# Kernel tuning notes

Measured on AMD Instinct MI355X. Metric: run time of the kernel, lower is better.

## Reference

```python
import jax, jax.numpy as jnp
import numpy as np

N = 100000      # num nodes
T = 4           # num edge types
E = 150000      # edges per edge type
HID = 128       # hidden_dim
NH = 8          # num_heads
D = 16          # per_head_dim
MS = NH * D     # message size


def setup_inputs() -> dict:
    key = jax.random.key(0)
    ks = jax.random.split(key, 6)
    x = jax.random.normal(ks[0], (N, HID), dtype=jnp.float32)
    adj = jax.random.randint(ks[1], (T, E, 2), 0, N, dtype=jnp.int32)
    Wq = jax.random.normal(ks[2], (T, HID, MS), dtype=jnp.float32) * 0.05
    Wk = jax.random.normal(ks[3], (T, HID, MS), dtype=jnp.float32) * 0.05
    Wm = jax.random.normal(ks[4], (T, 2 * HID, MS), dtype=jnp.float32) * 0.05
    bm = jnp.zeros((T, MS), dtype=jnp.float32)
    return {"x": x, "adj": adj, "Wq": Wq, "Wk": Wk, "Wm": Wm, "bm": bm}


def reference(x, adj, Wq, Wk, Wm, bm):
    scale = D ** (-0.5)
    srcs = adj[..., 0]  # [T, E]
    tgts = adj[..., 1]  # [T, E]
    xs = x[srcs]        # [T, E, HID] gather
    xt = x[tgts]        # [T, E, HID] gather
    # per-edge-type message MLP (depth 1 -> single linear + relu)
    feats = jnp.concatenate([xs, xt], axis=-1)                 # [T, E, 2*HID]
    msgs = jax.nn.relu(jnp.einsum('tef,tfm->tem', feats, Wm) + bm[:, None, :])
    msgs = msgs.reshape(T * E, NH, D)
    # per-edge-type Q/K projections and per-head dot-product scores
    q = (scale * jnp.einsum('teh,thm->tem', xt, Wq)).reshape(T * E, NH, D)
    k = jnp.einsum('teh,thm->tem', xs, Wk).reshape(T * E, NH, D)
    scores = jnp.einsum('ehd,ehd->eh', q, k)                   # [T*E, NH]
    idx = tgts.reshape(-1)                                     # [T*E]
    # segment (scatter) softmax over edges grouped by target node
    m = jax.ops.segment_max(scores, idx, num_segments=N)       # [N, NH]
    m = jnp.where(jnp.isfinite(m), m, jnp.zeros_like(m))       # empty segments
    e = jnp.exp(scores - m[idx])
    denom = jax.ops.segment_sum(e, idx, num_segments=N)        # [N, NH]
    probs = e / denom[idx]                                     # [T*E, NH]
    # weighted scatter-sum aggregation
    agg = jax.ops.segment_sum(probs[..., None] * msgs, idx, num_segments=N)
    return agg.reshape(N, MS)
```

## Files before the change

### kernel.cpp

```cpp
#include <hip/hip_runtime.h>
#include <hip/hip_bf16.h>
#include <cstdint>

#define NND 100000
#define NT 4
#define NE 150000
#define TOTE (NT * NE)
#define HID 128
#define NHD 8
#define MS 128
#define SEL ((size_t)NND * MS)
#define BAT 8
#define PNW 32

typedef __bf16 bf16x8 __attribute__((ext_vector_type(8)));
typedef float f32x4 __attribute__((ext_vector_type(4)));

__device__ __forceinline__ float bf2f(unsigned int u16) {
  unsigned int b = u16 << 16;
  return __builtin_bit_cast(float, b);
}
__device__ __forceinline__ unsigned short f2bf(float f) {
  unsigned int b = __builtin_bit_cast(unsigned int, f);
  b += 0x7FFFu + ((b >> 16) & 1u);
  return (unsigned short)(b >> 16);
}

__global__ void k_convert_x(const float* __restrict__ x, unsigned short* __restrict__ xb) {
  int i = (blockIdx.x * 256 + threadIdx.x) * 4;
  float4 v = *reinterpret_cast<const float4*>(x + i);
  ushort4 o;
  o.x = f2bf(v.x); o.y = f2bf(v.y); o.z = f2bf(v.z); o.w = f2bf(v.w);
  *reinterpret_cast<ushort4*>(xb + i) = o;
}

__global__ void k_pack_w(const float* __restrict__ Wq, const float* __restrict__ Wk,
                         const float* __restrict__ Wm, unsigned short* __restrict__ wp) {
  int p = blockIdx.x * 256 + threadIdx.x;
  int e    = p & 7;
  int lane = (p >> 3) & 63;
  int b    = (p >> 9) & 3;
  int c    = (p >> 11) & 7;
  int kind = (p >> 14) & 3;
  int t    = p >> 16;
  int col = c * 16 + (lane & 15);
  int k   = b * 32 + (lane >> 4) * 8 + e;
  float v;
  if (kind == 0)      v = 0.25f * Wq[((size_t)t * HID + k) * MS + col];
  else if (kind == 1) v = Wk[((size_t)t * HID + k) * MS + col];
  else if (kind == 2) v = Wm[((size_t)t * 2 * HID + k) * MS + col];
  else                v = Wm[((size_t)t * 2 * HID + HID + k) * MS + col];
  wp[p] = f2bf(v);
}

__global__ void k_hist(const int* __restrict__ adj, int* __restrict__ counts) {
  int i = blockIdx.x * 256 + threadIdx.x;
  if (i < TOTE) atomicAdd(&counts[adj[2 * i + 1]], 1);
}

__global__ void k_blocksum(const int* __restrict__ counts, int* __restrict__ bsum) {
  __shared__ int s[4];
  int i = blockIdx.x * 256 + threadIdx.x;
  int v = (i < NND) ? counts[i] : 0;
#pragma unroll
  for (int d = 1; d < 64; d <<= 1) v += __shfl_xor(v, d);
  if ((threadIdx.x & 63) == 0) s[threadIdx.x >> 6] = v;
  __syncthreads();
  if (threadIdx.x == 0) bsum[blockIdx.x] = s[0] + s[1] + s[2] + s[3];
}

__global__ void k_scan_mid(int* __restrict__ bsum, int nb, int* __restrict__ offsets) {
  __shared__ int s[512];
  int t = threadIdx.x;
  s[t] = (t < nb) ? bsum[t] : 0;
  __syncthreads();
  for (int d = 1; d < 512; d <<= 1) {
    int u = (t >= d) ? s[t - d] : 0;
    __syncthreads();
    s[t] += u;
    __syncthreads();
  }
  if (t < nb) bsum[t] = (t > 0) ? s[t - 1] : 0;
  if (t == 0) offsets[NND] = TOTE;
}

__global__ void k_scan_add(const int* __restrict__ counts, const int* __restrict__ bsum,
                           int* __restrict__ offsets, int* __restrict__ cursor) {
  __shared__ int s[256];
  int b = blockIdx.x, t = threadIdx.x, i = b * 256 + t;
  s[t] = (i < NND) ? counts[i] : 0;
  __syncthreads();
  for (int d = 1; d < 256; d <<= 1) {
    int u = (t >= d) ? s[t - d] : 0;
    __syncthreads();
    s[t] += u;
    __syncthreads();
  }
  int excl = ((t > 0) ? s[t - 1] : 0) + bsum[b];
  if (i < NND) { offsets[i] = excl; cursor[i] = excl; }
}

__global__ void k_scatter(const int* __restrict__ adj, int* __restrict__ cursor,
                          int* __restrict__ edata) {
  int i = blockIdx.x * 256 + threadIdx.x;
  if (i >= TOTE) return;
  int src = adj[2 * i], tgt = adj[2 * i + 1];
  int t = i / NE;
  int pos = atomicAdd(&cursor[tgt], 1);
  edata[pos] = src | (t << 24);
}

__global__ __launch_bounds__(256) void k_projF(const unsigned short* __restrict__ xb,
                                               const unsigned short* __restrict__ wp,
                                               unsigned short* __restrict__ bQ,
                                               unsigned short* __restrict__ bK,
                                               unsigned short* __restrict__ bMs,
                                               unsigned short* __restrict__ bMt,
                                               int tlo, int npass, int cpx) {
  __shared__ unsigned short wlds[16384];
  int flat = blockIdx.x;
  int xcd = flat & 7;
  int idx = flat >> 3;
  int chunk = xcd * cpx + idx / npass;
  int pass  = idx - (idx / npass) * npass;
  if (chunk * 128 >= NND) return;
  int tt = pass >> 2, kind = pass & 3;
  int wave = threadIdx.x >> 6;
  int lane = threadIdx.x & 63;
  int la = lane & 15, kg = lane >> 4;
  int nodeBase = chunk * 128 + wave * PNW;

  {
    const char* gsrc = (const char*)(wp + (size_t)((tlo + tt) * 4 + kind) * 16384) +
                       wave * 8192 + lane * 16;
    char* ldst = (char*)wlds + wave * 8192;
#pragma unroll
    for (int i = 0; i < 8; i++) {
      __builtin_amdgcn_global_load_lds(
          (const __attribute__((address_space(1))) unsigned int*)(gsrc + i * 1024),
          (__attribute__((address_space(3))) unsigned int*)(ldst + i * 1024), 16, 0, 0);
    }
  }

  bf16x8 xf[2][4];
#pragma unroll
  for (int g = 0; g < 2; g++) {
    int node = nodeBase + g * 16 + la;
    if (node < NND) {
      const unsigned short* ap = xb + (size_t)node * HID + kg * 8;
#pragma unroll
      for (int b = 0; b < 4; b++)
        xf[g][b] = *reinterpret_cast<const bf16x8*>(ap + b * 32);
    } else {
#pragma unroll
      for (int b = 0; b < 4; b++)
#pragma unroll
        for (int e = 0; e < 8; e++) xf[g][b][e] = (__bf16)0.0f;
    }
  }

  asm volatile("s_waitcnt vmcnt(0)");
  __syncthreads();

  f32x4 acc[2][8];
#pragma unroll
  for (int g = 0; g < 2; g++)
#pragma unroll
    for (int c = 0; c < 8; c++)
#pragma unroll
      for (int r = 0; r < 4; r++) acc[g][c][r] = 0.0f;

#pragma unroll
  for (int c = 0; c < 8; c++)
#pragma unroll
    for (int b = 0; b < 4; b++) {
      bf16x8 wf = *reinterpret_cast<const bf16x8*>(wlds + (c * 4 + b) * 512 + lane * 8);
      acc[0][c] = __builtin_amdgcn_mfma_f32_16x16x32_bf16(wf, xf[0][b], acc[0][c], 0, 0, 0);
      acc[1][c] = __builtin_amdgcn_mfma_f32_16x16x32_bf16(wf, xf[1][b], acc[1][c], 0, 0, 0);
    }

  __syncthreads();

  unsigned short* ob =
      (kind == 0 ? bQ : kind == 1 ? bK : kind == 2 ? bMs : bMt) + (size_t)tt * SEL;
#pragma unroll
  for (int g = 0; g < 2; g++) {
    char* rowp = (char*)wlds + (size_t)(wave * 32 + g * 16 + la) * 256;
    int sw = (la & 7) << 5;
#pragma unroll
    for (int c = 0; c < 8; c++) {
      uint2 o;
      o.x = (unsigned int)f2bf(acc[g][c][0]) | ((unsigned int)f2bf(acc[g][c][1]) << 16);
      o.y = (unsigned int)f2bf(acc[g][c][2]) | ((unsigned int)f2bf(acc[g][c][3]) << 16);
      *reinterpret_cast<uint2*>(rowp + ((c * 32 + kg * 8) ^ sw)) = o;
    }
  }
#pragma unroll
  for (int p = 0; p < 8; p++) {
    int nidx = p * 4 + kg;
    int node = nodeBase + nidx;
    char* rp = (char*)wlds + (size_t)(wave * 32 + nidx) * 256;
    uint4 v = *reinterpret_cast<uint4*>(rp + ((la * 16) ^ ((nidx & 7) << 5)));
    if (node < NND)
      *reinterpret_cast<uint4*>(ob + (size_t)node * MS + la * 8) = v;
  }
}

__global__ __launch_bounds__(256) void k_edge(const int* __restrict__ edata,
                                              const int* __restrict__ offsets,
                                              const unsigned short* __restrict__ qall,
                                              const unsigned short* __restrict__ kall,
                                              const unsigned short* __restrict__ msall,
                                              const unsigned short* __restrict__ mtall,
                                              const float* __restrict__ bm,
                                              float* __restrict__ out,
                                              float* __restrict__ denom,
                                              int tlo, int ntp, int init, int fin) {
  int wave = threadIdx.x >> 6, lane = threadIdx.x & 63;
  int n = blockIdx.x * 4 + wave;
  if (n >= NND) return;
  int beg = offsets[n], end = offsets[n + 1];
  int h = lane >> 3;

  unsigned int qv[NT] = {0, 0, 0, 0}, mtv[NT] = {0, 0, 0, 0};
  float2 bmv[NT];
#pragma unroll
  for (int tt = 0; tt < NT; tt++) {
    if (tt < ntp) {
      qv[tt]  = *reinterpret_cast<const unsigned int*>(qall  + ((size_t)tt * NND + n) * MS + lane * 2);
      mtv[tt] = *reinterpret_cast<const unsigned int*>(mtall + ((size_t)tt * NND + n) * MS + lane * 2);
      bmv[tt] = *reinterpret_cast<const float2*>(bm + (size_t)(tlo + tt) * MS + lane * 2);
    } else {
      bmv[tt] = make_float2(0.f, 0.f);
    }
  }

  float dsum = 0.0f, m0 = 0.0f, m1 = 0.0f;
  for (int base = beg; base < end; base += BAT) {
    int ed[BAT];
    unsigned int ku[BAT], mu[BAT];
#pragma unroll
    for (int j = 0; j < BAT; j++) {
      int p = base + j;
      ed[j] = (p < end) ? edata[p] : -1;
    }
#pragma unroll
    for (int j = 0; j < BAT; j++) {
      unsigned int rel = (((unsigned int)ed[j]) >> 24) - (unsigned int)tlo;
      bool ok = (ed[j] >= 0) && (rel < (unsigned int)ntp);
      size_t a = ((size_t)rel * NND + (ed[j] & 0xFFFFFF)) * MS + lane * 2;
      ku[j] = ok ? *reinterpret_cast<const unsigned int*>(kall + a) : 0u;
      mu[j] = ok ? *reinterpret_cast<const unsigned int*>(msall + a) : 0u;
    }
#pragma unroll
    for (int j = 0; j < BAT; j++) {
      unsigned int rel = (((unsigned int)ed[j]) >> 24) - (unsigned int)tlo;
      if ((ed[j] >= 0) && (rel < (unsigned int)ntp)) {
        unsigned int qu = rel == 0 ? qv[0] : rel == 1 ? qv[1] : rel == 2 ? qv[2] : qv[3];
        float part = bf2f(qu & 0xFFFFu) * bf2f(ku[j] & 0xFFFFu) +
                     bf2f(qu >> 16) * bf2f(ku[j] >> 16);
        part += __shfl_xor(part, 1);
        part += __shfl_xor(part, 2);
        part += __shfl_xor(part, 4);
        float ev = __expf(part);
        dsum += ev;
        unsigned int mtu = rel == 0 ? mtv[0] : rel == 1 ? mtv[1] : rel == 2 ? mtv[2] : mtv[3];
        float bx = rel == 0 ? bmv[0].x : rel == 1 ? bmv[1].x : rel == 2 ? bmv[2].x : bmv[3].x;
        float by = rel == 0 ? bmv[0].y : rel == 1 ? bmv[1].y : rel == 2 ? bmv[2].y : bmv[3].y;
        float a0 = bf2f(mu[j] & 0xFFFFu) + bf2f(mtu & 0xFFFFu) + bx;
        float a1 = bf2f(mu[j] >> 16) + bf2f(mtu >> 16) + by;
        m0 += ev * fmaxf(a0, 0.f);
        m1 += ev * fmaxf(a1, 0.f);
      }
    }
  }

  float* op = out + (size_t)n * MS + lane * 2;
  if (!init) {
    float2 prev = *reinterpret_cast<float2*>(op);
    m0 += prev.x; m1 += prev.y;
    dsum += denom[n * NHD + h];
  }
  if (fin) {
    float inv = dsum > 0.f ? 1.0f / dsum : 0.0f;
    float2 o; o.x = m0 * inv; o.y = m1 * inv;
    *reinterpret_cast<float2*>(op) = o;
  } else {
    float2 o; o.x = m0; o.y = m1;
    *reinterpret_cast<float2*>(op) = o;
    if ((lane & 7) == 0) denom[n * NHD + h] = dsum;
  }
}

extern "C" void kernel_launch(void* const* d_in, const int* in_sizes, int n_in,
                              void* d_out, int out_size, void* d_ws, size_t ws_size,
                              hipStream_t stream) {
  const float* x  = (const float*)d_in[0];
  const int* adj  = (const int*)d_in[1];
  const float* Wq = (const float*)d_in[2];
  const float* Wk = (const float*)d_in[3];
  const float* Wm = (const float*)d_in[4];
  const float* bm = (const float*)d_in[5];
  float* out = (float*)d_out;

  char* ws = (char*)d_ws;
  size_t off = 0;
  auto alloc = [&](size_t bytes) -> char* {
    char* p = ws + off;
    off += (bytes + 255) & ~(size_t)255;
    return p;
  };
  unsigned short* xb = (unsigned short*)alloc((size_t)NND * HID * 2);
  unsigned short* wp = (unsigned short*)alloc((size_t)NT * 4 * HID * MS * 2);
  int* counts   = (int*)alloc((size_t)NND * 4);
  int* offsets  = (int*)alloc((size_t)(NND + 1) * 4);
  int* cursor   = (int*)alloc((size_t)NND * 4);
  int* bsum     = (int*)alloc(512 * 4);
  int* edata    = (int*)alloc((size_t)TOTE * 4);
  float* denom  = (float*)alloc((size_t)NND * NHD * 4);

  size_t avail = (ws_size > off) ? (ws_size - off) : 0;
  const size_t perType = 4 * SEL * 2;
  int TPH = 1;
  if (avail >= 4 * perType)      TPH = 4;
  else if (avail >= 2 * perType) TPH = 2;
  unsigned short* region = (unsigned short*)(ws + off);
  unsigned short* bufQ  = region;
  unsigned short* bufK  = region + (size_t)TPH * SEL;
  unsigned short* bufMs = region + (size_t)2 * TPH * SEL;
  unsigned short* bufMt = region + (size_t)3 * TPH * SEL;

  hipMemsetAsync(counts, 0, (size_t)NND * 4, stream);

  k_convert_x<<<(NND * HID) / (256 * 4), 256, 0, stream>>>(x, xb);
  k_pack_w<<<(NT * 4 * HID * MS) / 256, 256, 0, stream>>>(Wq, Wk, Wm, wp);

  const int NB1 = (NND + 255) / 256;
  k_hist<<<(TOTE + 255) / 256, 256, 0, stream>>>(adj, counts);
  k_blocksum<<<NB1, 256, 0, stream>>>(counts, bsum);
  k_scan_mid<<<1, 512, 0, stream>>>(bsum, NB1, offsets);
  k_scan_add<<<NB1, 256, 0, stream>>>(counts, bsum, offsets, cursor);
  k_scatter<<<(TOTE + 255) / 256, 256, 0, stream>>>(adj, cursor, edata);

  const int nchunks = (NND + 127) / 128;
  const int cpx = (nchunks + 7) / 8;
  const int ngrid = (NND + 3) / 4;

  for (int tlo = 0; tlo < NT; tlo += TPH) {
    int npass = TPH * 4;
    int pgrid = 8 * cpx * npass;
    k_projF<<<pgrid, 256, 0, stream>>>(xb, wp, bufQ, bufK, bufMs, bufMt, tlo, npass, cpx);
    k_edge<<<ngrid, 256, 0, stream>>>(edata, offsets, bufQ, bufK, bufMs, bufMt, bm,
                                      out, denom, tlo, TPH,
                                      tlo == 0 ? 1 : 0, (tlo + TPH >= NT) ? 1 : 0);
  }
}
```

Before: 350.1 us.

## Bucket edges by type window and process two edges per wave in parallel

The CSR build now keys edges by (type window, target), so each edge pass reads only the edges belonging to the currently projected types instead of scanning and skipping the rest. The edge kernel splits each wave into two half-waves that handle alternating edges with 4 features per lane, then merges the partial sums with a cross-half shuffle. The TPH=1 fallback is dropped, so the scheme requires room for at least two types of projection buffers. The block-sum scan grows to a 1024-thread kernel to cover the larger count array.

```diff
diff --git a/kernel.cpp b/kernel.cpp
--- a/kernel.cpp
+++ b/kernel.cpp
@@ -10,7 +10,7 @@
 #define NHD 8
 #define MS 128
 #define SEL ((size_t)NND * MS)
-#define BAT 8
+#define BATP 4
 #define PNW 32
 
 typedef __bf16 bf16x8 __attribute__((ext_vector_type(8)));
@@ -53,15 +53,18 @@
   wp[p] = f2bf(v);
 }
 
-__global__ void k_hist(const int* __restrict__ adj, int* __restrict__ counts) {
+__global__ void k_hist(const int* __restrict__ adj, int* __restrict__ counts, int tshift) {
   int i = blockIdx.x * 256 + threadIdx.x;
-  if (i < TOTE) atomicAdd(&counts[adj[2 * i + 1]], 1);
-}
-
-__global__ void k_blocksum(const int* __restrict__ counts, int* __restrict__ bsum) {
+  if (i < TOTE) {
+    int win = (i / NE) >> tshift;
+    atomicAdd(&counts[win * NND + adj[2 * i + 1]], 1);
+  }
+}
+
+__global__ void k_blocksum(const int* __restrict__ counts, int* __restrict__ bsum, int ntot) {
   __shared__ int s[4];
   int i = blockIdx.x * 256 + threadIdx.x;
-  int v = (i < NND) ? counts[i] : 0;
+  int v = (i < ntot) ? counts[i] : 0;
 #pragma unroll
   for (int d = 1; d < 64; d <<= 1) v += __shfl_xor(v, d);
   if ((threadIdx.x & 63) == 0) s[threadIdx.x >> 6] = v;
@@ -69,26 +72,27 @@
   if (threadIdx.x == 0) bsum[blockIdx.x] = s[0] + s[1] + s[2] + s[3];
 }
 
-__global__ void k_scan_mid(int* __restrict__ bsum, int nb, int* __restrict__ offsets) {
-  __shared__ int s[512];
+__global__ void k_scan_mid(int* __restrict__ bsum, int nb, int* __restrict__ offsets,
+                           int ntot) {
+  __shared__ int s[1024];
   int t = threadIdx.x;
   s[t] = (t < nb) ? bsum[t] : 0;
   __syncthreads();
-  for (int d = 1; d < 512; d <<= 1) {
+  for (int d = 1; d < 1024; d <<= 1) {
     int u = (t >= d) ? s[t - d] : 0;
     __syncthreads();
     s[t] += u;
     __syncthreads();
   }
   if (t < nb) bsum[t] = (t > 0) ? s[t - 1] : 0;
-  if (t == 0) offsets[NND] = TOTE;
+  if (t == 0) offsets[ntot] = TOTE;
 }
 
 __global__ void k_scan_add(const int* __restrict__ counts, const int* __restrict__ bsum,
-                           int* __restrict__ offsets, int* __restrict__ cursor) {
+                           int* __restrict__ offsets, int* __restrict__ cursor, int ntot) {
   __shared__ int s[256];
   int b = blockIdx.x, t = threadIdx.x, i = b * 256 + t;
-  s[t] = (i < NND) ? counts[i] : 0;
+  s[t] = (i < ntot) ? counts[i] : 0;
   __syncthreads();
   for (int d = 1; d < 256; d <<= 1) {
     int u = (t >= d) ? s[t - d] : 0;
@@ -97,16 +101,17 @@
     __syncthreads();
   }
   int excl = ((t > 0) ? s[t - 1] : 0) + bsum[b];
-  if (i < NND) { offsets[i] = excl; cursor[i] = excl; }
+  if (i < ntot) { offsets[i] = excl; cursor[i] = excl; }
 }
 
 __global__ void k_scatter(const int* __restrict__ adj, int* __restrict__ cursor,
-                          int* __restrict__ edata) {
+                          int* __restrict__ edata, int tshift) {
   int i = blockIdx.x * 256 + threadIdx.x;
   if (i >= TOTE) return;
   int src = adj[2 * i], tgt = adj[2 * i + 1];
   int t = i / NE;
-  int pos = atomicAdd(&cursor[tgt], 1);
+  int win = t >> tshift;
+  int pos = atomicAdd(&cursor[win * NND + tgt], 1);
   edata[pos] = src | (t << 24);
 }
 
@@ -207,7 +212,7 @@
 }
 
 __global__ __launch_bounds__(256) void k_edge(const int* __restrict__ edata,
-                                              const int* __restrict__ offsets,
+                                              const int* __restrict__ offs,
                                               const unsigned short* __restrict__ qall,
                                               const unsigned short* __restrict__ kall,
                                               const unsigned short* __restrict__ msall,
@@ -219,76 +224,93 @@
   int wave = threadIdx.x >> 6, lane = threadIdx.x & 63;
   int n = blockIdx.x * 4 + wave;
   if (n >= NND) return;
-  int beg = offsets[n], end = offsets[n + 1];
-  int h = lane >> 3;
-
-  unsigned int qv[NT] = {0, 0, 0, 0}, mtv[NT] = {0, 0, 0, 0};
-  float2 bmv[NT];
+  int beg = offs[n], end = offs[n + 1];
+  int hw = lane >> 5;
+  int hl = lane & 31;
+
+  uint2 qv2[NT], mtv2[NT];
+  float4 bmv[NT];
 #pragma unroll
   for (int tt = 0; tt < NT; tt++) {
     if (tt < ntp) {
-      qv[tt]  = *reinterpret_cast<const unsigned int*>(qall  + ((size_t)tt * NND + n) * MS + lane * 2);
-      mtv[tt] = *reinterpret_cast<const unsigned int*>(mtall + ((size_t)tt * NND + n) * MS + lane * 2);
-      bmv[tt] = *reinterpret_cast<const float2*>(bm + (size_t)(tlo + tt) * MS + lane * 2);
+      qv2[tt]  = *reinterpret_cast<const uint2*>(qall  + ((size_t)tt * NND + n) * MS + hl * 4);
+      mtv2[tt] = *reinterpret_cast<const uint2*>(mtall + ((size_t)tt * NND + n) * MS + hl * 4);
+      bmv[tt]  = *reinterpret_cast<const float4*>(bm + (size_t)(tlo + tt) * MS + hl * 4);
     } else {
-      bmv[tt] = make_float2(0.f, 0.f);
-    }
-  }
-
-  float dsum = 0.0f, m0 = 0.0f, m1 = 0.0f;
-  for (int base = beg; base < end; base += BAT) {
-    int ed[BAT];
-    unsigned int ku[BAT], mu[BAT];
-#pragma unroll
-    for (int j = 0; j < BAT; j++) {
-      int p = base + j;
+      qv2[tt] = make_uint2(0, 0); mtv2[tt] = make_uint2(0, 0);
+      bmv[tt] = make_float4(0.f, 0.f, 0.f, 0.f);
+    }
+  }
+
+  float dsum = 0.0f, m0 = 0.0f, m1 = 0.0f, m2 = 0.0f, m3 = 0.0f;
+  for (int base = beg; base < end; base += 2 * BATP) {
+    int ed[BATP];
+    uint2 ku[BATP], mu[BATP];
+#pragma unroll
+    for (int j = 0; j < BATP; j++) {
+      int p = base + 2 * j + hw;
       ed[j] = (p < end) ? edata[p] : -1;
     }
 #pragma unroll
-    for (int j = 0; j < BAT; j++) {
+    for (int j = 0; j < BATP; j++) {
+      bool ok = ed[j] >= 0;
       unsigned int rel = (((unsigned int)ed[j]) >> 24) - (unsigned int)tlo;
-      bool ok = (ed[j] >= 0) && (rel < (unsigned int)ntp);
-      size_t a = ((size_t)rel * NND + (ed[j] & 0xFFFFFF)) * MS + lane * 2;
-      ku[j] = ok ? *reinterpret_cast<const unsigned int*>(kall + a) : 0u;
-      mu[j] = ok ? *reinterpret_cast<const unsigned int*>(msall + a) : 0u;
-    }
-#pragma unroll
-    for (int j = 0; j < BAT; j++) {
+      size_t a = ((size_t)(ok ? rel : 0u) * NND + (ed[j] & 0xFFFFFF)) * MS + hl * 4;
+      ku[j] = ok ? *reinterpret_cast<const uint2*>(kall + a) : make_uint2(0, 0);
+      mu[j] = ok ? *reinterpret_cast<const uint2*>(msall + a) : make_uint2(0, 0);
+    }
+#pragma unroll
+    for (int j = 0; j < BATP; j++) {
+      bool ok = ed[j] >= 0;
       unsigned int rel = (((unsigned int)ed[j]) >> 24) - (unsigned int)tlo;
-      if ((ed[j] >= 0) && (rel < (unsigned int)ntp)) {
-        unsigned int qu = rel == 0 ? qv[0] : rel == 1 ? qv[1] : rel == 2 ? qv[2] : qv[3];
-        float part = bf2f(qu & 0xFFFFu) * bf2f(ku[j] & 0xFFFFu) +
-                     bf2f(qu >> 16) * bf2f(ku[j] >> 16);
-        part += __shfl_xor(part, 1);
-        part += __shfl_xor(part, 2);
-        part += __shfl_xor(part, 4);
-        float ev = __expf(part);
-        dsum += ev;
-        unsigned int mtu = rel == 0 ? mtv[0] : rel == 1 ? mtv[1] : rel == 2 ? mtv[2] : mtv[3];
-        float bx = rel == 0 ? bmv[0].x : rel == 1 ? bmv[1].x : rel == 2 ? bmv[2].x : bmv[3].x;
-        float by = rel == 0 ? bmv[0].y : rel == 1 ? bmv[1].y : rel == 2 ? bmv[2].y : bmv[3].y;
-        float a0 = bf2f(mu[j] & 0xFFFFu) + bf2f(mtu & 0xFFFFu) + bx;
-        float a1 = bf2f(mu[j] >> 16) + bf2f(mtu >> 16) + by;
-        m0 += ev * fmaxf(a0, 0.f);
-        m1 += ev * fmaxf(a1, 0.f);
-      }
-    }
-  }
-
-  float* op = out + (size_t)n * MS + lane * 2;
+      uint2 qu  = rel == 0 ? qv2[0]  : rel == 1 ? qv2[1]  : rel == 2 ? qv2[2]  : qv2[3];
+      float part = bf2f(qu.x & 0xFFFFu) * bf2f(ku[j].x & 0xFFFFu) +
+                   bf2f(qu.x >> 16)     * bf2f(ku[j].x >> 16) +
+                   bf2f(qu.y & 0xFFFFu) * bf2f(ku[j].y & 0xFFFFu) +
+                   bf2f(qu.y >> 16)     * bf2f(ku[j].y >> 16);
+      part += __shfl_xor(part, 1);
+      part += __shfl_xor(part, 2);
+      float ev = ok ? __expf(part) : 0.0f;
+      dsum += ev;
+      uint2 mtu = rel == 0 ? mtv2[0] : rel == 1 ? mtv2[1] : rel == 2 ? mtv2[2] : mtv2[3];
+      float4 bv = rel == 0 ? bmv[0]  : rel == 1 ? bmv[1]  : rel == 2 ? bmv[2]  : bmv[3];
+      float a0 = bf2f(mu[j].x & 0xFFFFu) + bf2f(mtu.x & 0xFFFFu) + bv.x;
+      float a1 = bf2f(mu[j].x >> 16)     + bf2f(mtu.x >> 16)     + bv.y;
+      float a2 = bf2f(mu[j].y & 0xFFFFu) + bf2f(mtu.y & 0xFFFFu) + bv.z;
+      float a3 = bf2f(mu[j].y >> 16)     + bf2f(mtu.y >> 16)     + bv.w;
+      m0 += ev * fmaxf(a0, 0.f);
+      m1 += ev * fmaxf(a1, 0.f);
+      m2 += ev * fmaxf(a2, 0.f);
+      m3 += ev * fmaxf(a3, 0.f);
+    }
+  }
+
+  dsum += __shfl_xor(dsum, 32);
+  m0 += __shfl_xor(m0, 32);
+  m1 += __shfl_xor(m1, 32);
+  m2 += __shfl_xor(m2, 32);
+  m3 += __shfl_xor(m3, 32);
+
+  float* op = out + (size_t)n * MS + hl * 4;
   if (!init) {
-    float2 prev = *reinterpret_cast<float2*>(op);
-    m0 += prev.x; m1 += prev.y;
-    dsum += denom[n * NHD + h];
+    dsum += denom[n * NHD + (hl >> 2)];
+    if (hw == 0) {
+      float4 prev = *reinterpret_cast<float4*>(op);
+      m0 += prev.x; m1 += prev.y; m2 += prev.z; m3 += prev.w;
+    }
   }
   if (fin) {
     float inv = dsum > 0.f ? 1.0f / dsum : 0.0f;
-    float2 o; o.x = m0 * inv; o.y = m1 * inv;
-    *reinterpret_cast<float2*>(op) = o;
+    if (hw == 0) {
+      float4 o; o.x = m0 * inv; o.y = m1 * inv; o.z = m2 * inv; o.w = m3 * inv;
+      *reinterpret_cast<float4*>(op) = o;
+    }
   } else {
-    float2 o; o.x = m0; o.y = m1;
-    *reinterpret_cast<float2*>(op) = o;
-    if ((lane & 7) == 0) denom[n * NHD + h] = dsum;
+    if (hw == 0) {
+      float4 o; o.x = m0; o.y = m1; o.z = m2; o.w = m3;
+      *reinterpret_cast<float4*>(op) = o;
+      if ((hl & 3) == 0) denom[n * NHD + (hl >> 2)] = dsum;
+    }
   }
 }
 
@@ -312,46 +334,49 @@
   };
   unsigned short* xb = (unsigned short*)alloc((size_t)NND * HID * 2);
   unsigned short* wp = (unsigned short*)alloc((size_t)NT * 4 * HID * MS * 2);
-  int* counts   = (int*)alloc((size_t)NND * 4);
-  int* offsets  = (int*)alloc((size_t)(NND + 1) * 4);
-  int* cursor   = (int*)alloc((size_t)NND * 4);
-  int* bsum     = (int*)alloc(512 * 4);
+  int* counts   = (int*)alloc((size_t)2 * NND * 4);
+  int* offsets  = (int*)alloc((size_t)(2 * NND + 1) * 4);
+  int* cursor   = (int*)alloc((size_t)2 * NND * 4);
+  int* bsum     = (int*)alloc(1024 * 4);
   int* edata    = (int*)alloc((size_t)TOTE * 4);
   float* denom  = (float*)alloc((size_t)NND * NHD * 4);
 
   size_t avail = (ws_size > off) ? (ws_size - off) : 0;
   const size_t perType = 4 * SEL * 2;
-  int TPH = 1;
-  if (avail >= 4 * perType)      TPH = 4;
-  else if (avail >= 2 * perType) TPH = 2;
+  int TPH = (avail >= 4 * perType) ? 4 : 2;
+  int tshift = (TPH == 4) ? 2 : 1;
+  int NWIN = NT / TPH;
+  int ntot = NWIN * NND;
   unsigned short* region = (unsigned short*)(ws + off);
   unsigned short* bufQ  = region;
   unsigned short* bufK  = region + (size_t)TPH * SEL;
   unsigned short* bufMs = region + (size_t)2 * TPH * SEL;
   unsigned short* bufMt = region + (size_t)3 * TPH * SEL;
 
-  hipMemsetAsync(counts, 0, (size_t)NND * 4, stream);
+  hipMemsetAsync(counts, 0, (size_t)ntot * 4, stream);
 
   k_convert_x<<<(NND * HID) / (256 * 4), 256, 0, stream>>>(x, xb);
   k_pack_w<<<(NT * 4 * HID * MS) / 256, 256, 0, stream>>>(Wq, Wk, Wm, wp);
 
-  const int NB1 = (NND + 255) / 256;
-  k_hist<<<(TOTE + 255) / 256, 256, 0, stream>>>(adj, counts);
-  k_blocksum<<<NB1, 256, 0, stream>>>(counts, bsum);
-  k_scan_mid<<<1, 512, 0, stream>>>(bsum, NB1, offsets);
-  k_scan_add<<<NB1, 256, 0, stream>>>(counts, bsum, offsets, cursor);
-  k_scatter<<<(TOTE + 255) / 256, 256, 0, stream>>>(adj, cursor, edata);
+  const int NBS = (ntot + 255) / 256;
+  k_hist<<<(TOTE + 255) / 256, 256, 0, stream>>>(adj, counts, tshift);
+  k_blocksum<<<NBS, 256, 0, stream>>>(counts, bsum, ntot);
+  k_scan_mid<<<1, 1024, 0, stream>>>(bsum, NBS, offsets, ntot);
+  k_scan_add<<<NBS, 256, 0, stream>>>(counts, bsum, offsets, cursor, ntot);
+  k_scatter<<<(TOTE + 255) / 256, 256, 0, stream>>>(adj, cursor, edata, tshift);
 
   const int nchunks = (NND + 127) / 128;
   const int cpx = (nchunks + 7) / 8;
   const int ngrid = (NND + 3) / 4;
 
-  for (int tlo = 0; tlo < NT; tlo += TPH) {
+  for (int w = 0; w < NWIN; w++) {
+    int tlo = w * TPH;
     int npass = TPH * 4;
     int pgrid = 8 * cpx * npass;
     k_projF<<<pgrid, 256, 0, stream>>>(xb, wp, bufQ, bufK, bufMs, bufMt, tlo, npass, cpx);
-    k_edge<<<ngrid, 256, 0, stream>>>(edata, offsets, bufQ, bufK, bufMs, bufMt, bm,
+    k_edge<<<ngrid, 256, 0, stream>>>(edata, offsets + (size_t)w * NND,
+                                      bufQ, bufK, bufMs, bufMt, bm,
                                       out, denom, tlo, TPH,
-                                      tlo == 0 ? 1 : 0, (tlo + TPH >= NT) ? 1 : 0);
-  }
-}
+                                      w == 0 ? 1 : 0, (w == NWIN - 1) ? 1 : 0);
+  }
+}
```

New measurement: 918.7 us. +162.4%, slower.

## Partition CSR by edge-type window so each edge pass reads only its edges

Applied to the files above, without the earlier changes.

Builds a separate CSR segment per edge-type window (target node offsets indexed by window), so the per-window edge kernel only iterates over edges whose type is resident in the projection buffers. Previously every pass walked all incoming edges and filtered out other types. This doubles the count/offset arrays and uses a 1024-thread mid scan. It also removes the single-type-per-pass fallback, assuming the workspace fits at least two types.

```diff
diff --git a/kernel.cpp b/kernel.cpp
--- a/kernel.cpp
+++ b/kernel.cpp
@@ -53,15 +53,18 @@
   wp[p] = f2bf(v);
 }
 
-__global__ void k_hist(const int* __restrict__ adj, int* __restrict__ counts) {
+__global__ void k_hist(const int* __restrict__ adj, int* __restrict__ counts, int tshift) {
   int i = blockIdx.x * 256 + threadIdx.x;
-  if (i < TOTE) atomicAdd(&counts[adj[2 * i + 1]], 1);
-}
-
-__global__ void k_blocksum(const int* __restrict__ counts, int* __restrict__ bsum) {
+  if (i < TOTE) {
+    int win = (i / NE) >> tshift;
+    atomicAdd(&counts[win * NND + adj[2 * i + 1]], 1);
+  }
+}
+
+__global__ void k_blocksum(const int* __restrict__ counts, int* __restrict__ bsum, int ntot) {
   __shared__ int s[4];
   int i = blockIdx.x * 256 + threadIdx.x;
-  int v = (i < NND) ? counts[i] : 0;
+  int v = (i < ntot) ? counts[i] : 0;
 #pragma unroll
   for (int d = 1; d < 64; d <<= 1) v += __shfl_xor(v, d);
   if ((threadIdx.x & 63) == 0) s[threadIdx.x >> 6] = v;
@@ -69,26 +72,27 @@
   if (threadIdx.x == 0) bsum[blockIdx.x] = s[0] + s[1] + s[2] + s[3];
 }
 
-__global__ void k_scan_mid(int* __restrict__ bsum, int nb, int* __restrict__ offsets) {
-  __shared__ int s[512];
+__global__ void k_scan_mid(int* __restrict__ bsum, int nb, int* __restrict__ offsets,
+                           int ntot) {
+  __shared__ int s[1024];
   int t = threadIdx.x;
   s[t] = (t < nb) ? bsum[t] : 0;
   __syncthreads();
-  for (int d = 1; d < 512; d <<= 1) {
+  for (int d = 1; d < 1024; d <<= 1) {
     int u = (t >= d) ? s[t - d] : 0;
     __syncthreads();
     s[t] += u;
     __syncthreads();
   }
   if (t < nb) bsum[t] = (t > 0) ? s[t - 1] : 0;
-  if (t == 0) offsets[NND] = TOTE;
+  if (t == 0) offsets[ntot] = TOTE;
 }
 
 __global__ void k_scan_add(const int* __restrict__ counts, const int* __restrict__ bsum,
-                           int* __restrict__ offsets, int* __restrict__ cursor) {
+                           int* __restrict__ offsets, int* __restrict__ cursor, int ntot) {
   __shared__ int s[256];
   int b = blockIdx.x, t = threadIdx.x, i = b * 256 + t;
-  s[t] = (i < NND) ? counts[i] : 0;
+  s[t] = (i < ntot) ? counts[i] : 0;
   __syncthreads();
   for (int d = 1; d < 256; d <<= 1) {
     int u = (t >= d) ? s[t - d] : 0;
@@ -97,16 +101,17 @@
     __syncthreads();
   }
   int excl = ((t > 0) ? s[t - 1] : 0) + bsum[b];
-  if (i < NND) { offsets[i] = excl; cursor[i] = excl; }
+  if (i < ntot) { offsets[i] = excl; cursor[i] = excl; }
 }
 
 __global__ void k_scatter(const int* __restrict__ adj, int* __restrict__ cursor,
-                          int* __restrict__ edata) {
+                          int* __restrict__ edata, int tshift) {
   int i = blockIdx.x * 256 + threadIdx.x;
   if (i >= TOTE) return;
   int src = adj[2 * i], tgt = adj[2 * i + 1];
   int t = i / NE;
-  int pos = atomicAdd(&cursor[tgt], 1);
+  int win = t >> tshift;
+  int pos = atomicAdd(&cursor[win * NND + tgt], 1);
   edata[pos] = src | (t << 24);
 }
 
@@ -207,7 +212,7 @@
 }
 
 __global__ __launch_bounds__(256) void k_edge(const int* __restrict__ edata,
-                                              const int* __restrict__ offsets,
+                                              const int* __restrict__ offs,
                                               const unsigned short* __restrict__ qall,
                                               const unsigned short* __restrict__ kall,
                                               const unsigned short* __restrict__ msall,
@@ -219,7 +224,7 @@
   int wave = threadIdx.x >> 6, lane = threadIdx.x & 63;
   int n = blockIdx.x * 4 + wave;
   if (n >= NND) return;
-  int beg = offsets[n], end = offsets[n + 1];
+  int beg = offs[n], end = offs[n + 1];
   int h = lane >> 3;
 
   unsigned int qv[NT] = {0, 0, 0, 0}, mtv[NT] = {0, 0, 0, 0};
@@ -246,16 +251,17 @@
     }
 #pragma unroll
     for (int j = 0; j < BAT; j++) {
-      unsigned int rel = (((unsigned int)ed[j]) >> 24) - (unsigned int)tlo;
-      bool ok = (ed[j] >= 0) && (rel < (unsigned int)ntp);
-      size_t a = ((size_t)rel * NND + (ed[j] & 0xFFFFFF)) * MS + lane * 2;
+      bool ok = ed[j] >= 0;
+      unsigned int rel = ok ? ((((unsigned int)ed[j]) >> 24) - (unsigned int)tlo) : 0u;
+      unsigned int src = ok ? ((unsigned int)ed[j] & 0xFFFFFFu) : 0u;
+      size_t a = ((size_t)rel * NND + src) * MS + lane * 2;
       ku[j] = ok ? *reinterpret_cast<const unsigned int*>(kall + a) : 0u;
       mu[j] = ok ? *reinterpret_cast<const unsigned int*>(msall + a) : 0u;
     }
 #pragma unroll
     for (int j = 0; j < BAT; j++) {
-      unsigned int rel = (((unsigned int)ed[j]) >> 24) - (unsigned int)tlo;
-      if ((ed[j] >= 0) && (rel < (unsigned int)ntp)) {
+      if (ed[j] >= 0) {
+        unsigned int rel = (((unsigned int)ed[j]) >> 24) - (unsigned int)tlo;
         unsigned int qu = rel == 0 ? qv[0] : rel == 1 ? qv[1] : rel == 2 ? qv[2] : qv[3];
         float part = bf2f(qu & 0xFFFFu) * bf2f(ku[j] & 0xFFFFu) +
                      bf2f(qu >> 16) * bf2f(ku[j] >> 16);
@@ -312,46 +318,49 @@
   };
   unsigned short* xb = (unsigned short*)alloc((size_t)NND * HID * 2);
   unsigned short* wp = (unsigned short*)alloc((size_t)NT * 4 * HID * MS * 2);
-  int* counts   = (int*)alloc((size_t)NND * 4);
-  int* offsets  = (int*)alloc((size_t)(NND + 1) * 4);
-  int* cursor   = (int*)alloc((size_t)NND * 4);
-  int* bsum     = (int*)alloc(512 * 4);
+  int* counts   = (int*)alloc((size_t)2 * NND * 4);
+  int* offsets  = (int*)alloc((size_t)(2 * NND + 1) * 4);
+  int* cursor   = (int*)alloc((size_t)2 * NND * 4);
+  int* bsum     = (int*)alloc(1024 * 4);
   int* edata    = (int*)alloc((size_t)TOTE * 4);
   float* denom  = (float*)alloc((size_t)NND * NHD * 4);
 
   size_t avail = (ws_size > off) ? (ws_size - off) : 0;
   const size_t perType = 4 * SEL * 2;
-  int TPH = 1;
-  if (avail >= 4 * perType)      TPH = 4;
-  else if (avail >= 2 * perType) TPH = 2;
+  int TPH = (avail >= 4 * perType) ? 4 : 2;
+  int tshift = (TPH == 4) ? 2 : 1;
+  int NWIN = NT / TPH;
+  int ntot = NWIN * NND;
   unsigned short* region = (unsigned short*)(ws + off);
   unsigned short* bufQ  = region;
   unsigned short* bufK  = region + (size_t)TPH * SEL;
   unsigned short* bufMs = region + (size_t)2 * TPH * SEL;
   unsigned short* bufMt = region + (size_t)3 * TPH * SEL;
 
-  hipMemsetAsync(counts, 0, (size_t)NND * 4, stream);
+  hipMemsetAsync(counts, 0, (size_t)ntot * 4, stream);
 
   k_convert_x<<<(NND * HID) / (256 * 4), 256, 0, stream>>>(x, xb);
   k_pack_w<<<(NT * 4 * HID * MS) / 256, 256, 0, stream>>>(Wq, Wk, Wm, wp);
 
-  const int NB1 = (NND + 255) / 256;
-  k_hist<<<(TOTE + 255) / 256, 256, 0, stream>>>(adj, counts);
-  k_blocksum<<<NB1, 256, 0, stream>>>(counts, bsum);
-  k_scan_mid<<<1, 512, 0, stream>>>(bsum, NB1, offsets);
-  k_scan_add<<<NB1, 256, 0, stream>>>(counts, bsum, offsets, cursor);
-  k_scatter<<<(TOTE + 255) / 256, 256, 0, stream>>>(adj, cursor, edata);
+  const int NBS = (ntot + 255) / 256;
+  k_hist<<<(TOTE + 255) / 256, 256, 0, stream>>>(adj, counts, tshift);
+  k_blocksum<<<NBS, 256, 0, stream>>>(counts, bsum, ntot);
+  k_scan_mid<<<1, 1024, 0, stream>>>(bsum, NBS, offsets, ntot);
+  k_scan_add<<<NBS, 256, 0, stream>>>(counts, bsum, offsets, cursor, ntot);
+  k_scatter<<<(TOTE + 255) / 256, 256, 0, stream>>>(adj, cursor, edata, tshift);
 
   const int nchunks = (NND + 127) / 128;
   const int cpx = (nchunks + 7) / 8;
   const int ngrid = (NND + 3) / 4;
 
-  for (int tlo = 0; tlo < NT; tlo += TPH) {
+  for (int w = 0; w < NWIN; w++) {
+    int tlo = w * TPH;
     int npass = TPH * 4;
     int pgrid = 8 * cpx * npass;
     k_projF<<<pgrid, 256, 0, stream>>>(xb, wp, bufQ, bufK, bufMs, bufMt, tlo, npass, cpx);
-    k_edge<<<ngrid, 256, 0, stream>>>(edata, offsets, bufQ, bufK, bufMs, bufMt, bm,
+    k_edge<<<ngrid, 256, 0, stream>>>(edata, offsets + (size_t)w * NND,
+                                      bufQ, bufK, bufMs, bufMt, bm,
                                       out, denom, tlo, TPH,
-                                      tlo == 0 ? 1 : 0, (tlo + TPH >= NT) ? 1 : 0);
-  }
-}
+                                      w == 0 ? 1 : 0, (w == NWIN - 1) ? 1 : 0);
+  }
+}
```

Measured after the change: 340.5 us. -2.8%, faster.
